# Performance work log

Hardware: AMD Instinct MI355X
Metric: run time of the kernel (lower is better)

The kernel has to match this reference:

```python
import jax, jax.numpy as jnp
import numpy as np

# Dim order: [N, K, C, P, Q, R, S]; memory levels: [L0_Registers, L1_Accumulator, L2_Scratchpad, L3_DRAM]
# Tensor types: 0=Input(N,C,P,Q) 1=Weight(K,C,R,S) 2=Output(N,K,P,Q)
DIM_MASK = jnp.array([[1,0,1,1,1,0,0],
                      [0,1,1,0,0,1,1],
                      [1,1,0,1,1,0,0]], dtype=bool)
# reuse dims: Input->K, Weight->N,P,Q, Output->C,R,S
REUSE_MASK = jnp.array([[0,1,0,0,0,0,0],
                        [1,0,0,1,1,0,0],
                        [0,0,1,0,0,1,1]], dtype=bool)

BYTES = 4.0
CLK_MHZ = 1000.0
DRAM_BW_GB_S = 100.0
PE_MAC_EPA_PJ = 0.56
L0_REG_EPA_PJ = 0.18
L1_BASE_EPA_PJ = 0.52
L1_COEFF_PJ_KB = 0.01
L2_BASE_EPA_PJ = 1.2
L2_COEFF_PJ_KB = 0.002
AREA_PER_PE = 0.01
AREA_PER_KB = 0.005

G = 500000  # number of (unfused) layers / fusion groups


def setup_inputs() -> dict:
    key = jax.random.key(0)
    k1, k2 = jax.random.split(key)
    temporal = 1.0 + jax.random.uniform(k1, (G, 7, 4), dtype=jnp.float32)
    spatial = 1.0 + jax.random.uniform(k2, (G, 7, 4), dtype=jnp.float32)
    return {
        "temporal_factors": temporal,
        "spatial_factors": spatial,
        "num_pes": jnp.array([256.0], dtype=jnp.float32),
        "buffer_sizes_kb": jnp.array([1.0, 64.0, 512.0], dtype=jnp.float32),  # L0, L1, L2
    }


def _masked_prod(x, mask):
    # x: [G,7,L], mask: [3,7] -> [G,3,L] product over masked dims
    return jnp.prod(jnp.where(mask[None, :, :, None], x[:, None, :, :], 1.0), axis=2)


def reference(temporal_factors, spatial_factors, num_pes, buffer_sizes_kb):
    pe = num_pes[0]
    sq = jnp.sqrt(pe)

    cumTS = jnp.cumprod(temporal_factors * spatial_factors, axis=2)  # prefix prod over levels
    cumT = jnp.cumprod(temporal_factors, axis=2)
    sufT = jnp.flip(jnp.cumprod(jnp.flip(temporal_factors, 2), 2), 2)  # suffix prod over levels

    macs = jnp.prod(cumTS[:, :, -1], axis=1)  # [G] product of full dim sizes

    fp = _masked_prod(cumTS, DIM_MASK)      # [G,3,4] data footprint up to level l
    outer = _masked_prod(sufT, DIM_MASK)    # [G,3,4] outer iterations from level l up
    ru = _masked_prod(cumT, REUSE_MASK)     # [G,3,4] reuse factor up to level l

    # interfaces (upper->lower): L3->L2, L2->L1, L1->L0
    low = jnp.array([2, 1, 0])
    up = jnp.array([3, 2, 1])
    acc = (fp[:, :, low] * (outer[:, :, up] / (ru[:, :, low] + 1e-9)) * BYTES).sum(axis=1)  # [G,3]

    # latency
    onchip_bw = 2.0 * sq * BYTES * CLK_MHZ * 1e6 / 1e9
    bw = jnp.stack([jnp.full((), DRAM_BW_GB_S), onchip_bw, onchip_bw])  # upper level bw per interface
    mem_lat = acc / (bw[None, :] * 1e9 + 1e-9)
    comp_lat = macs / (pe * CLK_MHZ * 1e6 + 1e-9)
    total_latency = jnp.maximum(comp_lat, mem_lat.max(axis=1)).sum()

    # energy (per interface, keyed by lower level: L2, L1, L0)
    epa = jnp.stack([
        L2_BASE_EPA_PJ + L2_COEFF_PJ_KB * buffer_sizes_kb[2],
        L1_BASE_EPA_PJ + L1_COEFF_PJ_KB * (buffer_sizes_kb[1] / sq),
        jnp.full((), L0_REG_EPA_PJ),
    ])
    total_energy = (macs * PE_MAC_EPA_PJ).sum() + ((acc / 4.0) @ epa).sum()

    # buffer mismatch for buffer levels L0, L1, L2
    req_kb = fp[:, :, :3].sum(axis=1) * BYTES / 1024.0  # [G,3]
    deficit = jax.nn.relu(req_kb - buffer_sizes_kb[None, :])
    total_mismatch = (deficit ** 2).sum()

    area = pe * AREA_PER_PE + (buffer_sizes_kb * AREA_PER_KB).sum()
    return (total_latency, total_energy, area, total_mismatch)
```

## Files before the change

### kernel.cpp

```cpp
#include <hip/hip_runtime.h>
#include <hip/hip_bf16.h>


typedef const __attribute__((address_space(1))) void* gptr_t;
typedef __attribute__((address_space(3))) void* lptr_t;

__global__ __launch_bounds__(256) void hpm_main(
    const float* __restrict__ T, const float* __restrict__ S,
    const float* __restrict__ PE, const float* __restrict__ BUF,
    double* __restrict__ part, int G, int NB)
{
    __shared__ float ldsT[7168];
    __shared__ float ldsS[7168];

    const int tid = threadIdx.x;
    const int g0  = blockIdx.x * 256;
    const int g   = g0 + tid;
    const bool full = (g0 + 256 <= G);

    float4 tv[7], sv[7];
    bool have = false;

    if (full) {
        const int wid = tid >> 6;
        const float* gT = T + (size_t)g0 * 28;
        const float* gS = S + (size_t)g0 * 28;
        #pragma unroll
        for (int k = 0; k < 7; ++k) {
            const int fidx = k * 256 + tid;
            const int uoff = (k * 256 + wid * 64) * 4;
            __builtin_amdgcn_global_load_lds((gptr_t)(gT + (size_t)fidx * 4),
                                             (lptr_t)&ldsT[uoff], 16, 0, 0);
            __builtin_amdgcn_global_load_lds((gptr_t)(gS + (size_t)fidx * 4),
                                             (lptr_t)&ldsS[uoff], 16, 0, 0);
        }
        __syncthreads();

        const float4* Tl = reinterpret_cast<const float4*>(&ldsT[tid * 28]);
        const float4* Sl = reinterpret_cast<const float4*>(&ldsS[tid * 28]);
        #pragma unroll
        for (int d = 0; d < 7; ++d) { tv[d] = Tl[d]; sv[d] = Sl[d]; }
        have = true;
    } else if (g < G) {
        const float4* Tp = reinterpret_cast<const float4*>(T) + (size_t)g * 7;
        const float4* Sp = reinterpret_cast<const float4*>(S) + (size_t)g * 7;
        #pragma unroll
        for (int d = 0; d < 7; ++d) { tv[d] = Tp[d]; sv[d] = Sp[d]; }
        have = true;
    }

    double lat = 0.0, en = 0.0, mis = 0.0;

    if (have) {
        const float pe = PE[0];
        const float sq = sqrtf(pe);
        const float b0 = BUF[0], b1 = BUF[1], b2 = BUF[2];

        float fpI[3] = {1.f,1.f,1.f}, fpW[3] = {1.f,1.f,1.f}, fpO[3] = {1.f,1.f,1.f};
        float otI[3] = {1.f,1.f,1.f}, otW[3] = {1.f,1.f,1.f}, otO[3] = {1.f,1.f,1.f};
        float ruI[3] = {1.f,1.f,1.f}, ruW[3] = {1.f,1.f,1.f}, ruO[3] = {1.f,1.f,1.f};
        float macs = 1.f;

        constexpr unsigned IN_D = 0x1D, WT_D = 0x66, OU_D = 0x1B;
        constexpr unsigned IN_R = 0x02, WT_R = 0x19, OU_R = 0x64;

        #pragma unroll
        for (int d = 0; d < 7; ++d) {
            const float4 t = tv[d];
            const float4 s = sv[d];

            const float ct0 = t.x;
            const float ct1 = ct0 * t.y;
            const float ct2 = ct1 * t.z;
            const float u0 = t.x * s.x, u1 = t.y * s.y, u2 = t.z * s.z, u3 = t.w * s.w;
            const float cs0 = u0;
            const float cs1 = cs0 * u1;
            const float cs2 = cs1 * u2;
            const float cs3 = cs2 * u3;
            const float st3 = t.w;
            const float st2 = t.z * st3;
            const float st1 = t.y * st2;

            macs *= cs3;

            if ((IN_D >> d) & 1) {
                fpI[0] *= cs0; fpI[1] *= cs1; fpI[2] *= cs2;
                otI[0] *= st1; otI[1] *= st2; otI[2] *= st3;
            }
            if ((WT_D >> d) & 1) {
                fpW[0] *= cs0; fpW[1] *= cs1; fpW[2] *= cs2;
                otW[0] *= st1; otW[1] *= st2; otW[2] *= st3;
            }
            if ((OU_D >> d) & 1) {
                fpO[0] *= cs0; fpO[1] *= cs1; fpO[2] *= cs2;
                otO[0] *= st1; otO[1] *= st2; otO[2] *= st3;
            }
            if ((IN_R >> d) & 1) { ruI[0] *= ct0; ruI[1] *= ct1; ruI[2] *= ct2; }
            if ((WT_R >> d) & 1) { ruW[0] *= ct0; ruW[1] *= ct1; ruW[2] *= ct2; }
            if ((OU_R >> d) & 1) { ruO[0] *= ct0; ruO[1] *= ct1; ruO[2] *= ct2; }
        }

        const float acc0 = 4.f * ( fpI[2] * otI[2] / (ruI[2] + 1e-9f)
                                 + fpW[2] * otW[2] / (ruW[2] + 1e-9f)
                                 + fpO[2] * otO[2] / (ruO[2] + 1e-9f) );
        const float acc1 = 4.f * ( fpI[1] * otI[1] / (ruI[1] + 1e-9f)
                                 + fpW[1] * otW[1] / (ruW[1] + 1e-9f)
                                 + fpO[1] * otO[1] / (ruO[1] + 1e-9f) );
        const float acc2 = 4.f * ( fpI[0] * otI[0] / (ruI[0] + 1e-9f)
                                 + fpW[0] * otW[0] / (ruW[0] + 1e-9f)
                                 + fpO[0] * otO[0] / (ruO[0] + 1e-9f) );

        const float bw_dram   = 100.0f * 1e9f + 1e-9f;
        const float bw_onchip = sq * 8e9f + 1e-9f;
        const float ml = fmaxf(acc0 / bw_dram,
                               fmaxf(acc1, acc2) / bw_onchip);
        const float cl = macs / (pe * 1e9f + 1e-9f);
        lat = (double)fmaxf(cl, ml);

        const float epa0 = 1.2f  + 0.002f * b2;
        const float epa1 = 0.52f + 0.01f  * (b1 / sq);
        const float epa2 = 0.18f;
        en = (double)(macs * 0.56f + (acc0 * epa0 + acc1 * epa1 + acc2 * epa2) * 0.25f);

        const float c = 4.f / 1024.f;
        const float r0 = (fpI[0] + fpW[0] + fpO[0]) * c;
        const float r1 = (fpI[1] + fpW[1] + fpO[1]) * c;
        const float r2 = (fpI[2] + fpW[2] + fpO[2]) * c;
        const float d0 = fmaxf(r0 - b0, 0.f);
        const float d1 = fmaxf(r1 - b1, 0.f);
        const float d2 = fmaxf(r2 - b2, 0.f);
        mis = (double)d0 * d0 + (double)d1 * d1 + (double)d2 * d2;
    }

    #pragma unroll
    for (int off = 32; off > 0; off >>= 1) {
        lat += __shfl_down(lat, off);
        en  += __shfl_down(en,  off);
        mis += __shfl_down(mis, off);
    }

    __shared__ double sred[3][4];
    const int wid  = threadIdx.x >> 6;
    const int lane = threadIdx.x & 63;
    if (lane == 0) { sred[0][wid] = lat; sred[1][wid] = en; sred[2][wid] = mis; }
    __syncthreads();

    if (threadIdx.x == 0) {
        double L = 0.0, E = 0.0, M = 0.0;
        #pragma unroll
        for (int w = 0; w < 4; ++w) { L += sred[0][w]; E += sred[1][w]; M += sred[2][w]; }
        part[0 * NB + blockIdx.x] = L;
        part[1 * NB + blockIdx.x] = E;
        part[2 * NB + blockIdx.x] = M;
    }
}

__global__ __launch_bounds__(256) void hpm_final(
    const double* __restrict__ part, int NB,
    const float* __restrict__ PE, const float* __restrict__ BUF,
    float* __restrict__ out)
{
    const int tid = threadIdx.x;
    double L = 0.0, E = 0.0, M = 0.0;
    for (int i = tid; i < NB; i += 256) {
        L += part[0 * NB + i];
        E += part[1 * NB + i];
        M += part[2 * NB + i];
    }

    #pragma unroll
    for (int off = 32; off > 0; off >>= 1) {
        L += __shfl_down(L, off);
        E += __shfl_down(E, off);
        M += __shfl_down(M, off);
    }

    __shared__ double sred[3][4];
    const int wid  = tid >> 6;
    const int lane = tid & 63;
    if (lane == 0) { sred[0][wid] = L; sred[1][wid] = E; sred[2][wid] = M; }
    __syncthreads();

    if (tid == 0) {
        double Lt = 0.0, Et = 0.0, Mt = 0.0;
        #pragma unroll
        for (int w = 0; w < 4; ++w) { Lt += sred[0][w]; Et += sred[1][w]; Mt += sred[2][w]; }
        out[0] = (float)Lt;
        out[1] = (float)Et;
        out[2] = PE[0] * 0.01f + (BUF[0] + BUF[1] + BUF[2]) * 0.005f;
        out[3] = (float)Mt;
    }
}

extern "C" void kernel_launch(void* const* d_in, const int* in_sizes, int n_in,
                              void* d_out, int out_size, void* d_ws, size_t ws_size,
                              hipStream_t stream) {
    const float* T   = (const float*)d_in[0];
    const float* S   = (const float*)d_in[1];
    const float* PE  = (const float*)d_in[2];
    const float* BUF = (const float*)d_in[3];
    float* out = (float*)d_out;
    double* ws = (double*)d_ws;

    const int G = in_sizes[0] / 28;
    const int blocks = (G + 255) / 256;

    hipLaunchKernelGGL(hpm_main, dim3(blocks), dim3(256), 0, stream,
                       T, S, PE, BUF, ws, G, blocks);
    hipLaunchKernelGGL(hpm_final, dim3(1), dim3(256), 0, stream,
                       ws, blocks, PE, BUF, out);
}
```

Measured before the change: 28.28 us.

## Use persistent grid with prefetched LDS tiles overlapping compute

Replaces the one-block-per-tile launch (about 1954 blocks) with a fixed grid of 512 persistent blocks that loop over tiles. Each block issues the async global-to-LDS load for its next tile after consuming the current one, so the load overlaps with the arithmetic. Constants are hoisted out of the loop and the final reduction reads a fixed 512 partials. The cost is two barriers per tile, a single LDS buffer that limits overlap, and possibly fewer resident waves to hide memory latency.

```diff
diff --git a/kernel.cpp b/kernel.cpp
--- a/kernel.cpp
+++ b/kernel.cpp
@@ -5,167 +5,189 @@
 typedef const __attribute__((address_space(1))) void* gptr_t;
 typedef __attribute__((address_space(3))) void* lptr_t;
 
-__global__ __launch_bounds__(256) void hpm_main(
+#define BLK 256
+#define NBK 512
+
+__global__ __launch_bounds__(BLK) void hpm_main(
     const float* __restrict__ T, const float* __restrict__ S,
     const float* __restrict__ PE, const float* __restrict__ BUF,
-    double* __restrict__ part, int G, int NB)
+    double* __restrict__ part, int G)
 {
-    __shared__ float ldsT[7168];
-    __shared__ float ldsS[7168];
+    __shared__ float ldsT[BLK * 28];
+    __shared__ float ldsS[BLK * 28];
 
     const int tid = threadIdx.x;
-    const int g0  = blockIdx.x * 256;
-    const int g   = g0 + tid;
-    const bool full = (g0 + 256 <= G);
-
-    float4 tv[7], sv[7];
-    bool have = false;
-
-    if (full) {
-        const int wid = tid >> 6;
-        const float* gT = T + (size_t)g0 * 28;
-        const float* gS = S + (size_t)g0 * 28;
+    const int wid = tid >> 6;
+    const int NT  = (G + BLK - 1) / BLK;
+
+    const float pe = PE[0];
+    const float sq = sqrtf(pe);
+    const float b0 = BUF[0], b1 = BUF[1], b2 = BUF[2];
+    const float bw_dram   = 100.0f * 1e9f + 1e-9f;
+    const float bw_onchip = sq * 8e9f + 1e-9f;
+    const float epa0 = 1.2f  + 0.002f * b2;
+    const float epa1 = 0.52f + 0.01f  * (b1 / sq);
+    const float epa2 = 0.18f;
+    const float inv_pe = 1.0f / (pe * 1e9f + 1e-9f);
+
+    auto issue_dma = [&](int t) {
+        const float* gT = T + (size_t)t * BLK * 28;
+        const float* gS = S + (size_t)t * BLK * 28;
         #pragma unroll
         for (int k = 0; k < 7; ++k) {
-            const int fidx = k * 256 + tid;
-            const int uoff = (k * 256 + wid * 64) * 4;
+            const int fidx = k * BLK + tid;
+            const int uoff = (k * BLK + wid * 64) * 4;
             __builtin_amdgcn_global_load_lds((gptr_t)(gT + (size_t)fidx * 4),
                                              (lptr_t)&ldsT[uoff], 16, 0, 0);
             __builtin_amdgcn_global_load_lds((gptr_t)(gS + (size_t)fidx * 4),
                                              (lptr_t)&ldsS[uoff], 16, 0, 0);
         }
+    };
+
+    double latA = 0.0, enA = 0.0, misA = 0.0;
+
+    {
+        const int t0 = blockIdx.x;
+        if (t0 < NT && t0 * BLK + BLK <= G) issue_dma(t0);
+    }
+
+    for (int t = blockIdx.x; t < NT; t += NBK) {
+        const bool full = (t * BLK + BLK <= G);
+        const int  g    = t * BLK + tid;
+
+        float4 tv[7], sv[7];
+        bool have = false;
+
         __syncthreads();
 
-        const float4* Tl = reinterpret_cast<const float4*>(&ldsT[tid * 28]);
-        const float4* Sl = reinterpret_cast<const float4*>(&ldsS[tid * 28]);
-        #pragma unroll
-        for (int d = 0; d < 7; ++d) { tv[d] = Tl[d]; sv[d] = Sl[d]; }
-        have = true;
-    } else if (g < G) {
-        const float4* Tp = reinterpret_cast<const float4*>(T) + (size_t)g * 7;
-        const float4* Sp = reinterpret_cast<const float4*>(S) + (size_t)g * 7;
-        #pragma unroll
-        for (int d = 0; d < 7; ++d) { tv[d] = Tp[d]; sv[d] = Sp[d]; }
-        have = true;
-    }
-
-    double lat = 0.0, en = 0.0, mis = 0.0;
-
-    if (have) {
-        const float pe = PE[0];
-        const float sq = sqrtf(pe);
-        const float b0 = BUF[0], b1 = BUF[1], b2 = BUF[2];
-
-        float fpI[3] = {1.f,1.f,1.f}, fpW[3] = {1.f,1.f,1.f}, fpO[3] = {1.f,1.f,1.f};
-        float otI[3] = {1.f,1.f,1.f}, otW[3] = {1.f,1.f,1.f}, otO[3] = {1.f,1.f,1.f};
-        float ruI[3] = {1.f,1.f,1.f}, ruW[3] = {1.f,1.f,1.f}, ruO[3] = {1.f,1.f,1.f};
-        float macs = 1.f;
-
-        constexpr unsigned IN_D = 0x1D, WT_D = 0x66, OU_D = 0x1B;
-        constexpr unsigned IN_R = 0x02, WT_R = 0x19, OU_R = 0x64;
-
-        #pragma unroll
-        for (int d = 0; d < 7; ++d) {
-            const float4 t = tv[d];
-            const float4 s = sv[d];
-
-            const float ct0 = t.x;
-            const float ct1 = ct0 * t.y;
-            const float ct2 = ct1 * t.z;
-            const float u0 = t.x * s.x, u1 = t.y * s.y, u2 = t.z * s.z, u3 = t.w * s.w;
-            const float cs0 = u0;
-            const float cs1 = cs0 * u1;
-            const float cs2 = cs1 * u2;
-            const float cs3 = cs2 * u3;
-            const float st3 = t.w;
-            const float st2 = t.z * st3;
-            const float st1 = t.y * st2;
-
-            macs *= cs3;
-
-            if ((IN_D >> d) & 1) {
-                fpI[0] *= cs0; fpI[1] *= cs1; fpI[2] *= cs2;
-                otI[0] *= st1; otI[1] *= st2; otI[2] *= st3;
+        if (full) {
+            const float4* Tl = reinterpret_cast<const float4*>(&ldsT[tid * 28]);
+            const float4* Sl = reinterpret_cast<const float4*>(&ldsS[tid * 28]);
+            #pragma unroll
+            for (int d = 0; d < 7; ++d) { tv[d] = Tl[d]; sv[d] = Sl[d]; }
+            have = true;
+        } else if (g < G) {
+            const float4* Tp = reinterpret_cast<const float4*>(T) + (size_t)g * 7;
+            const float4* Sp = reinterpret_cast<const float4*>(S) + (size_t)g * 7;
+            #pragma unroll
+            for (int d = 0; d < 7; ++d) { tv[d] = Tp[d]; sv[d] = Sp[d]; }
+            have = true;
+        }
+
+        __syncthreads();
+
+        {
+            const int tn = t + NBK;
+            if (tn < NT && tn * BLK + BLK <= G) issue_dma(tn);
+        }
+
+        if (have) {
+            float fpI[3] = {1.f,1.f,1.f}, fpW[3] = {1.f,1.f,1.f}, fpO[3] = {1.f,1.f,1.f};
+            float otI[3] = {1.f,1.f,1.f}, otW[3] = {1.f,1.f,1.f}, otO[3] = {1.f,1.f,1.f};
+            float ruI[3] = {1.f,1.f,1.f}, ruW[3] = {1.f,1.f,1.f}, ruO[3] = {1.f,1.f,1.f};
+            float macs = 1.f;
+
+            constexpr unsigned IN_D = 0x1D, WT_D = 0x66, OU_D = 0x1B;
+            constexpr unsigned IN_R = 0x02, WT_R = 0x19, OU_R = 0x64;
+
+            #pragma unroll
+            for (int d = 0; d < 7; ++d) {
+                const float4 tt = tv[d];
+                const float4 ss = sv[d];
+
+                const float ct0 = tt.x;
+                const float ct1 = ct0 * tt.y;
+                const float ct2 = ct1 * tt.z;
+                const float u0 = tt.x * ss.x, u1 = tt.y * ss.y;
+                const float u2 = tt.z * ss.z, u3 = tt.w * ss.w;
+                const float cs0 = u0;
+                const float cs1 = cs0 * u1;
+                const float cs2 = cs1 * u2;
+                const float cs3 = cs2 * u3;
+                const float st3 = tt.w;
+                const float st2 = tt.z * st3;
+                const float st1 = tt.y * st2;
+
+                macs *= cs3;
+
+                if ((IN_D >> d) & 1) {
+                    fpI[0] *= cs0; fpI[1] *= cs1; fpI[2] *= cs2;
+                    otI[0] *= st1; otI[1] *= st2; otI[2] *= st3;
+                }
+                if ((WT_D >> d) & 1) {
+                    fpW[0] *= cs0; fpW[1] *= cs1; fpW[2] *= cs2;
+                    otW[0] *= st1; otW[1] *= st2; otW[2] *= st3;
+                }
+                if ((OU_D >> d) & 1) {
+                    fpO[0] *= cs0; fpO[1] *= cs1; fpO[2] *= cs2;
+                    otO[0] *= st1; otO[1] *= st2; otO[2] *= st3;
+                }
+                if ((IN_R >> d) & 1) { ruI[0] *= ct0; ruI[1] *= ct1; ruI[2] *= ct2; }
+                if ((WT_R >> d) & 1) { ruW[0] *= ct0; ruW[1] *= ct1; ruW[2] *= ct2; }
+                if ((OU_R >> d) & 1) { ruO[0] *= ct0; ruO[1] *= ct1; ruO[2] *= ct2; }
             }
-            if ((WT_D >> d) & 1) {
-                fpW[0] *= cs0; fpW[1] *= cs1; fpW[2] *= cs2;
-                otW[0] *= st1; otW[1] *= st2; otW[2] *= st3;
-            }
-            if ((OU_D >> d) & 1) {
-                fpO[0] *= cs0; fpO[1] *= cs1; fpO[2] *= cs2;
-                otO[0] *= st1; otO[1] *= st2; otO[2] *= st3;
-            }
-            if ((IN_R >> d) & 1) { ruI[0] *= ct0; ruI[1] *= ct1; ruI[2] *= ct2; }
-            if ((WT_R >> d) & 1) { ruW[0] *= ct0; ruW[1] *= ct1; ruW[2] *= ct2; }
-            if ((OU_R >> d) & 1) { ruO[0] *= ct0; ruO[1] *= ct1; ruO[2] *= ct2; }
-        }
-
-        const float acc0 = 4.f * ( fpI[2] * otI[2] / (ruI[2] + 1e-9f)
-                                 + fpW[2] * otW[2] / (ruW[2] + 1e-9f)
-                                 + fpO[2] * otO[2] / (ruO[2] + 1e-9f) );
-        const float acc1 = 4.f * ( fpI[1] * otI[1] / (ruI[1] + 1e-9f)
-                                 + fpW[1] * otW[1] / (ruW[1] + 1e-9f)
-                                 + fpO[1] * otO[1] / (ruO[1] + 1e-9f) );
-        const float acc2 = 4.f * ( fpI[0] * otI[0] / (ruI[0] + 1e-9f)
-                                 + fpW[0] * otW[0] / (ruW[0] + 1e-9f)
-                                 + fpO[0] * otO[0] / (ruO[0] + 1e-9f) );
-
-        const float bw_dram   = 100.0f * 1e9f + 1e-9f;
-        const float bw_onchip = sq * 8e9f + 1e-9f;
-        const float ml = fmaxf(acc0 / bw_dram,
-                               fmaxf(acc1, acc2) / bw_onchip);
-        const float cl = macs / (pe * 1e9f + 1e-9f);
-        lat = (double)fmaxf(cl, ml);
-
-        const float epa0 = 1.2f  + 0.002f * b2;
-        const float epa1 = 0.52f + 0.01f  * (b1 / sq);
-        const float epa2 = 0.18f;
-        en = (double)(macs * 0.56f + (acc0 * epa0 + acc1 * epa1 + acc2 * epa2) * 0.25f);
-
-        const float c = 4.f / 1024.f;
-        const float r0 = (fpI[0] + fpW[0] + fpO[0]) * c;
-        const float r1 = (fpI[1] + fpW[1] + fpO[1]) * c;
-        const float r2 = (fpI[2] + fpW[2] + fpO[2]) * c;
-        const float d0 = fmaxf(r0 - b0, 0.f);
-        const float d1 = fmaxf(r1 - b1, 0.f);
-        const float d2 = fmaxf(r2 - b2, 0.f);
-        mis = (double)d0 * d0 + (double)d1 * d1 + (double)d2 * d2;
+
+            const float acc0 = 4.f * ( fpI[2] * otI[2] / (ruI[2] + 1e-9f)
+                                     + fpW[2] * otW[2] / (ruW[2] + 1e-9f)
+                                     + fpO[2] * otO[2] / (ruO[2] + 1e-9f) );
+            const float acc1 = 4.f * ( fpI[1] * otI[1] / (ruI[1] + 1e-9f)
+                                     + fpW[1] * otW[1] / (ruW[1] + 1e-9f)
+                                     + fpO[1] * otO[1] / (ruO[1] + 1e-9f) );
+            const float acc2 = 4.f * ( fpI[0] * otI[0] / (ruI[0] + 1e-9f)
+                                     + fpW[0] * otW[0] / (ruW[0] + 1e-9f)
+                                     + fpO[0] * otO[0] / (ruO[0] + 1e-9f) );
+
+            const float ml = fmaxf(acc0 / bw_dram, fmaxf(acc1, acc2) / bw_onchip);
+            const float cl = macs * inv_pe;
+            latA += (double)fmaxf(cl, ml);
+
+            enA += (double)(macs * 0.56f + (acc0 * epa0 + acc1 * epa1 + acc2 * epa2) * 0.25f);
+
+            const float c = 4.f / 1024.f;
+            const float r0 = (fpI[0] + fpW[0] + fpO[0]) * c;
+            const float r1 = (fpI[1] + fpW[1] + fpO[1]) * c;
+            const float r2 = (fpI[2] + fpW[2] + fpO[2]) * c;
+            const float d0 = fmaxf(r0 - b0, 0.f);
+            const float d1 = fmaxf(r1 - b1, 0.f);
+            const float d2 = fmaxf(r2 - b2, 0.f);
+            misA += (double)d0 * d0 + (double)d1 * d1 + (double)d2 * d2;
+        }
     }
 
     #pragma unroll
     for (int off = 32; off > 0; off >>= 1) {
-        lat += __shfl_down(lat, off);
-        en  += __shfl_down(en,  off);
-        mis += __shfl_down(mis, off);
+        latA += __shfl_down(latA, off);
+        enA  += __shfl_down(enA,  off);
+        misA += __shfl_down(misA, off);
     }
 
     __shared__ double sred[3][4];
-    const int wid  = threadIdx.x >> 6;
-    const int lane = threadIdx.x & 63;
-    if (lane == 0) { sred[0][wid] = lat; sred[1][wid] = en; sred[2][wid] = mis; }
+    const int lane = tid & 63;
+    if (lane == 0) { sred[0][wid] = latA; sred[1][wid] = enA; sred[2][wid] = misA; }
     __syncthreads();
 
-    if (threadIdx.x == 0) {
+    if (tid == 0) {
         double L = 0.0, E = 0.0, M = 0.0;
         #pragma unroll
         for (int w = 0; w < 4; ++w) { L += sred[0][w]; E += sred[1][w]; M += sred[2][w]; }
-        part[0 * NB + blockIdx.x] = L;
-        part[1 * NB + blockIdx.x] = E;
-        part[2 * NB + blockIdx.x] = M;
+        part[0 * NBK + blockIdx.x] = L;
+        part[1 * NBK + blockIdx.x] = E;
+        part[2 * NBK + blockIdx.x] = M;
     }
 }
 
 __global__ __launch_bounds__(256) void hpm_final(
-    const double* __restrict__ part, int NB,
+    const double* __restrict__ part,
     const float* __restrict__ PE, const float* __restrict__ BUF,
     float* __restrict__ out)
 {
     const int tid = threadIdx.x;
     double L = 0.0, E = 0.0, M = 0.0;
-    for (int i = tid; i < NB; i += 256) {
-        L += part[0 * NB + i];
-        E += part[1 * NB + i];
-        M += part[2 * NB + i];
+    #pragma unroll
+    for (int i = tid; i < NBK; i += 256) {
+        L += part[0 * NBK + i];
+        E += part[1 * NBK + i];
+        M += part[2 * NBK + i];
     }
 
     #pragma unroll
@@ -203,10 +225,9 @@
     double* ws = (double*)d_ws;
 
     const int G = in_sizes[0] / 28;
-    const int blocks = (G + 255) / 256;
-
-    hipLaunchKernelGGL(hpm_main, dim3(blocks), dim3(256), 0, stream,
-                       T, S, PE, BUF, ws, G, blocks);
+
+    hipLaunchKernelGGL(hpm_main, dim3(NBK), dim3(BLK), 0, stream,
+                       T, S, PE, BUF, ws, G);
     hipLaunchKernelGGL(hpm_final, dim3(1), dim3(256), 0, stream,
-                       ws, blocks, PE, BUF, out);
+                       ws, PE, BUF, out);
 }
```

Result: faster. 26.52 us (-6.2%).
